# Performance work log

Measured on AMD Instinct MI355X. Metric: run time of the kernel, lower is better.

Reference implementation:

```python
import jax, jax.numpy as jnp
import numpy as np

HASH_PRIME = 5099  # primes[layer_id=0]
MIN_CAPACITY = 4


def setup_inputs() -> dict:
    key = jax.random.key(0)
    k1, k2, k3, k4, k5 = jax.random.split(key, 5)
    B, T, D, F, E = 8, 4096, 512, 1792, 64
    x = jax.random.normal(k1, (B, T, D), dtype=jnp.float32)
    token_ids = jax.random.randint(k2, (B, T), 0, 50257, dtype=jnp.int32)
    # Expert params stacked over E (random instead of the degenerate zero init)
    Wk = jax.random.normal(k3, (E, F, D), dtype=jnp.float32) * 0.02
    Wr = jax.random.normal(k4, (E, D, D), dtype=jnp.float32) * 0.02
    Wv = jax.random.normal(k5, (E, D, F), dtype=jnp.float32) * 0.02
    return {"x": x, "token_ids": token_ids, "Wk": Wk, "Wr": Wr, "Wv": Wv}


def reference(x, token_ids, Wk, Wr, Wv):
    B, T, D = x.shape
    E = Wk.shape[0]
    S = B * T
    # capacity_factor = 1, k = 1 -> capacity = ceil(S / E), at least min_capacity
    cap = max(MIN_CAPACITY, -(-S // E))

    tid = token_ids.reshape(S)
    e_idx = (tid % HASH_PRIME) % E                     # hash routing, top-1, gate weight 1.0

    onehot = jax.nn.one_hot(e_idx, E, dtype=jnp.int32)  # [S, E]
    rank = (jnp.cumsum(onehot, axis=0) * onehot).sum(axis=1)  # 1-based rank within expert
    pos = rank - 1                                      # slot index within expert
    kept = pos < cap                                    # capacity drop (first-come order)

    xf = x.reshape(S, D)
    pos_safe = jnp.where(kept, pos, cap)                # out-of-bounds -> dropped by scatter
    dispatched = jnp.zeros((E, cap, D), x.dtype).at[e_idx, pos_safe].set(xf, mode='drop')

    # RWKV expert FFN, batched over experts
    h = jnp.square(jax.nn.relu(jnp.einsum('ecd,efd->ecf', dispatched, Wk)))  # [E,C,F]
    kv = jnp.einsum('ecf,edf->ecd', h, Wv)                                   # [E,C,D]
    r = jax.nn.sigmoid(jnp.einsum('ecd,egd->ecg', dispatched, Wr))           # [E,C,D]
    expert_out = r * kv

    # combine: gather each token's slot; dropped tokens get zeros
    yf = expert_out[e_idx, jnp.minimum(pos, cap - 1)] * kept[:, None].astype(x.dtype)
    return yf.reshape(B, T, D)
```

## Files before the change

### kernel.cpp

```cpp
#include <hip/hip_runtime.h>
#include <hip/hip_fp16.h>

#define HASH_PRIME 5099
#define NE 64
#define ND 512
#define NF 1792
#define NS 32768
#define CAP 512

typedef unsigned short u16;
typedef __attribute__((ext_vector_type(8))) short bf16x8;
typedef __attribute__((ext_vector_type(4))) float f32x4;

__device__ __forceinline__ u16 f2bf(float f) {
  union { float f; unsigned u; } v; v.f = f;
  return (u16)((v.u + 0x7FFFu + ((v.u >> 16) & 1u)) >> 16);
}
__device__ __forceinline__ unsigned pkbf2(float a, float b) {
  return (unsigned)f2bf(a) | ((unsigned)f2bf(b) << 16);
}

__device__ __forceinline__ void gld16(const void* g, void* l) {
  __builtin_amdgcn_global_load_lds(
      (const __attribute__((address_space(1))) unsigned int*)(uintptr_t)g,
      (__attribute__((address_space(3))) unsigned int*)(uintptr_t)l,
      16, 0, 0);
}

__global__ __launch_bounds__(512) void route1(const int* __restrict__ tok,
                                              int* __restrict__ rank_local,
                                              int* __restrict__ hist) {
  __shared__ int se[512];
  __shared__ int h[NE];
  int b = blockIdx.x, t = threadIdx.x;
  int s = b * 512 + t;
  int e = (tok[s] % HASH_PRIME) % NE;
  se[t] = e;
  if (t < NE) h[t] = 0;
  __syncthreads();
  int cnt = 0;
  for (int j = 0; j < t; ++j) cnt += (se[j] == e);
  rank_local[s] = cnt;
  atomicAdd(&h[e], 1);
  __syncthreads();
  if (t < NE) hist[b * NE + t] = h[t];
}

__global__ __launch_bounds__(512) void route2(const int* __restrict__ tok,
                                              const int* __restrict__ rank_local,
                                              const int* __restrict__ hist,
                                              int* __restrict__ slot_src) {
  __shared__ int off[NE];
  int b = blockIdx.x, t = threadIdx.x;
  if (t < NE) {
    int o = 0;
    for (int bb = 0; bb < b; ++bb) o += hist[bb * NE + t];
    off[t] = o;
  }
  __syncthreads();
  int s = b * 512 + t;
  int e = (tok[s] % HASH_PRIME) % NE;
  int pos = off[e] + rank_local[s];
  if (pos < CAP) slot_src[e * CAP + pos] = s;
}

__global__ __launch_bounds__(256) void dispatchx(const float* __restrict__ x,
                                                 const int* __restrict__ slot_src,
                                                 u16* __restrict__ Xd) {
  int b = blockIdx.x;
  int t = threadIdx.x;
  int row = b * 4 + (t >> 6);
  int col = (t & 63) * 8;
  int s = slot_src[row];
  uint4 w = make_uint4(0u, 0u, 0u, 0u);
  if (s >= 0) {
    const float4* p = (const float4*)(x + (size_t)s * ND + col);
    float4 a = p[0], c = p[1];
    w.x = pkbf2(a.x, a.y); w.y = pkbf2(a.z, a.w);
    w.z = pkbf2(c.x, c.y); w.w = pkbf2(c.z, c.w);
  }
  *(uint4*)(Xd + (size_t)row * ND + col) = w;
}


#define GDECL \
  __shared__ u16 As[2][256 * 32]; \
  __shared__ u16 Bs[2][128 * 32]; \
  const int t = threadIdx.x; \
  const int l = t & 63; \
  const int w = t >> 6; \
  const int wm = w >> 1; \
  const int wn = w & 1; \
  const int lrow = l & 15; \
  const int swz = ((l >> 4) ^ ((l >> 1) & 3)) * 8; \
  const int ra_row = t >> 2; \
  const int ra_col = ((t & 3) ^ ((t >> 3) & 3)) * 8; \
  const int brow = t >> 2; \
  const int bseg = t & 3; \
  const int wb_idx = brow * 32 + (((t & 3) ^ ((t >> 3) & 3)) * 8);

#define INIT_ACC do { \
  _Pragma("unroll") for (int m_ = 0; m_ < 4; ++m_) \
    _Pragma("unroll") for (int n_ = 0; n_ < 4; ++n_) \
      acc[m_][n_] = (f32x4){0.f, 0.f, 0.f, 0.f}; \
} while (0)

#define ISSUE_A(buf, ks, abase, astride) do { \
  const u16* g_ = (abase) + (size_t)ra_row * (astride) + (ks) * 32 + ra_col; \
  gld16(g_, (char*)As[buf] + t * 16); \
  gld16(g_ + (size_t)128 * (astride), (char*)As[buf] + t * 16 + 8192); \
} while (0)

#define LOAD_B(ks, bbase, bstride) do { \
  const float4* p_ = (const float4*)((bbase) + (size_t)brow * (bstride) + (ks) * 32 + bseg * 8); \
  fb0 = p_[0]; fb1 = p_[1]; \
} while (0)

#define WRITE_B(buf) do { \
  uint4 wv_; \
  wv_.x = pkbf2(fb0.x, fb0.y); wv_.y = pkbf2(fb0.z, fb0.w); \
  wv_.z = pkbf2(fb1.x, fb1.y); wv_.w = pkbf2(fb1.z, fb1.w); \
  *(uint4*)&Bs[buf][wb_idx] = wv_; \
} while (0)

#define COMPUTE(buf) do { \
  bf16x8 af_[4], bf_[4]; \
  _Pragma("unroll") for (int m_ = 0; m_ < 4; ++m_) \
    af_[m_] = *(const bf16x8*)&As[buf][(wm * 64 + m_ * 16 + lrow) * 32 + swz]; \
  _Pragma("unroll") for (int n_ = 0; n_ < 4; ++n_) \
    bf_[n_] = *(const bf16x8*)&Bs[buf][(wn * 64 + n_ * 16 + lrow) * 32 + swz]; \
  _Pragma("unroll") for (int m_ = 0; m_ < 4; ++m_) \
    _Pragma("unroll") for (int n_ = 0; n_ < 4; ++n_) \
      acc[m_][n_] = __builtin_amdgcn_mfma_f32_16x16x32_bf16(af_[m_], bf_[n_], acc[m_][n_], 0, 0, 0); \
} while (0)

#define GEMM_LOOP(NK, abase, astride, bbase, bstride) do { \
  float4 fb0, fb1; \
  ISSUE_A(0, 0, abase, astride); \
  LOAD_B(0, bbase, bstride); \
  WRITE_B(0); \
  __syncthreads(); \
  _Pragma("unroll 2") \
  for (int ks = 0; ks < (NK); ++ks) { \
    const int cur = ks & 1; \
    if (ks + 1 < (NK)) { \
      ISSUE_A(cur ^ 1, ks + 1, abase, astride); \
      LOAD_B(ks + 1, bbase, bstride); \
    } \
    COMPUTE(cur); \
    if (ks + 1 < (NK)) WRITE_B(cur ^ 1); \
    __syncthreads(); \
  } \
} while (0)

__global__ __launch_bounds__(512, 4) void g1(const u16* __restrict__ Xd,
                                             const float* __restrict__ Wk,
                                             u16* __restrict__ H) {
  GDECL
  const int wg = (blockIdx.x & 7) * (1792 / 8) + (blockIdx.x >> 3);
  const int e = wg / 28, rem = wg % 28;
  const int n0 = (rem >> 1) * 128;
  const int m0 = (rem & 1) * 256;
  f32x4 acc[4][4];
  INIT_ACC;
  const u16*  abase = Xd + ((size_t)e * CAP + m0) * ND;
  const float* bbase = Wk + ((size_t)e * NF + n0) * ND;
  GEMM_LOOP(16, abase, ND, bbase, ND);

  #pragma unroll
  for (int m = 0; m < 4; ++m) {
    #pragma unroll
    for (int i = 0; i < 4; ++i) {
      int r = m0 + wm * 64 + m * 16 + (l >> 4) * 4 + i;
      size_t base = ((size_t)e * CAP + r) * NF + n0 + wn * 64 + lrow;
      #pragma unroll
      for (int n = 0; n < 4; ++n) {
        float v = acc[m][n][i];
        v = v > 0.f ? v * v : 0.f;
        H[base + n * 16] = f2bf(v);
      }
    }
  }
}

__global__ __launch_bounds__(512, 4) void g2a(const u16* __restrict__ Xd,
                                              const float* __restrict__ Wr,
                                              __half* __restrict__ R) {
  GDECL
  const int wg = (blockIdx.x & 7) * (512 / 8) + (blockIdx.x >> 3);
  const int e = wg / 8, rem = wg % 8;
  const int n0 = (rem >> 1) * 128;
  const int m0 = (rem & 1) * 256;
  f32x4 acc[4][4];
  INIT_ACC;
  const u16*  abase = Xd + ((size_t)e * CAP + m0) * ND;
  const float* bbase = Wr + ((size_t)e * ND + n0) * ND;
  GEMM_LOOP(16, abase, ND, bbase, ND);

  #pragma unroll
  for (int m = 0; m < 4; ++m) {
    #pragma unroll
    for (int i = 0; i < 4; ++i) {
      int r = m0 + wm * 64 + m * 16 + (l >> 4) * 4 + i;
      size_t base = ((size_t)e * CAP + r) * ND + n0 + wn * 64 + lrow;
      #pragma unroll
      for (int n = 0; n < 4; ++n) {
        float s = 1.f / (1.f + __expf(-acc[m][n][i]));
        R[base + n * 16] = __float2half(s);
      }
    }
  }
}

__global__ __launch_bounds__(512, 4) void g2b(const u16* __restrict__ H,
                                              const float* __restrict__ Wv,
                                              const __half* __restrict__ R,
                                              const int* __restrict__ slot_src,
                                              float* __restrict__ out) {
  GDECL
  __shared__ int ss[256];
  const int wg = (blockIdx.x & 7) * (512 / 8) + (blockIdx.x >> 3);
  const int e = wg / 8, rem = wg % 8;
  const int n0 = (rem >> 1) * 128;
  const int m0 = (rem & 1) * 256;
  if (t < 256) ss[t] = slot_src[e * CAP + m0 + t];
  f32x4 acc[4][4];
  INIT_ACC;
  const u16*  abase = H  + ((size_t)e * CAP + m0) * NF;
  const float* bbase = Wv + ((size_t)e * ND + n0) * NF;
  GEMM_LOOP(56, abase, NF, bbase, NF);

  #pragma unroll
  for (int m = 0; m < 4; ++m) {
    #pragma unroll
    for (int i = 0; i < 4; ++i) {
      int rl = wm * 64 + m * 16 + (l >> 4) * 4 + i;
      int s = ss[rl];
      if (s >= 0) {
        const __half* rp = R + ((size_t)e * CAP + m0 + rl) * ND + n0 + wn * 64 + lrow;
        float* op = out + (size_t)s * ND + n0 + wn * 64 + lrow;
        #pragma unroll
        for (int n = 0; n < 4; ++n) {
          op[n * 16] = __half2float(rp[n * 16]) * acc[m][n][i];
        }
      }
    }
  }
}

extern "C" void kernel_launch(void* const* d_in, const int* in_sizes, int n_in,
                              void* d_out, int out_size, void* d_ws, size_t ws_size,
                              hipStream_t stream) {
  const float* x   = (const float*)d_in[0];
  const int*   tok = (const int*)d_in[1];
  const float* Wk  = (const float*)d_in[2];
  const float* Wr  = (const float*)d_in[3];
  const float* Wv  = (const float*)d_in[4];
  float* out = (float*)d_out;

  char* ws = (char*)d_ws;
  int*    slot_src   = (int*)ws;
  int*    rank_local = (int*)(ws + 131072);
  int*    hist       = (int*)(ws + 262144);
  u16*    Xd         = (u16*)(ws + (1 << 20));
  __half* R          = (__half*)(ws + 34603008);
  u16*    H          = (u16*)(ws + 68157440);

  (void)hipMemsetAsync(d_out, 0, (size_t)out_size * sizeof(float), stream);
  (void)hipMemsetAsync(slot_src, 0xFF, NE * CAP * sizeof(int), stream);
  route1<<<64, 512, 0, stream>>>(tok, rank_local, hist);
  route2<<<64, 512, 0, stream>>>(tok, rank_local, hist, slot_src);
  dispatchx<<<NS / 4, 256, 0, stream>>>(x, slot_src, Xd);
  g1 <<<1792, 512, 0, stream>>>(Xd, Wk, H);
  g2a<<<512,  512, 0, stream>>>(Xd, Wr, R);
  g2b<<<512,  512, 0, stream>>>(H, Wv, R, slot_src, out);
}
```

Measured before the change: 343.5 us.

## Fuse receptance GEMM into value GEMM and shrink GEMM tiles to 128x128

Merges the Wr sigmoid GEMM into the Wv GEMM kernel. The sigmoid gate is kept packed as fp16 in registers, so the R intermediate is never written to or reread from global memory, and one launch is removed. Tiles change from 256x128 with 512 threads to 128x128 with 256 threads, with each thread loading 16 B-floats, which doubles the block counts. The trade-off is higher register pressure from holding the gate values across the second GEMM, plus more redundant weight loads because of the smaller M tiles.

```diff
diff --git a/kernel.cpp b/kernel.cpp
--- a/kernel.cpp
+++ b/kernel.cpp
@@ -18,6 +18,14 @@
 }
 __device__ __forceinline__ unsigned pkbf2(float a, float b) {
   return (unsigned)f2bf(a) | ((unsigned)f2bf(b) << 16);
+}
+__device__ __forceinline__ unsigned pkh2(float a, float b) {
+  __half2 h = __floats2half2_rn(a, b);
+  return __builtin_bit_cast(unsigned, h);
+}
+__device__ __forceinline__ float uph(unsigned w, int hi) {
+  __half2 h = __builtin_bit_cast(__half2, w);
+  return hi ? __high2float(h) : __low2float(h);
 }
 
 __device__ __forceinline__ void gld16(const void* g, void* l) {
@@ -84,7 +92,7 @@
 
 
 #define GDECL \
-  __shared__ u16 As[2][256 * 32]; \
+  __shared__ u16 As[2][128 * 32]; \
   __shared__ u16 Bs[2][128 * 32]; \
   const int t = threadIdx.x; \
   const int l = t & 63; \
@@ -95,9 +103,10 @@
   const int swz = ((l >> 4) ^ ((l >> 1) & 3)) * 8; \
   const int ra_row = t >> 2; \
   const int ra_col = ((t & 3) ^ ((t >> 3) & 3)) * 8; \
-  const int brow = t >> 2; \
-  const int bseg = t & 3; \
-  const int wb_idx = brow * 32 + (((t & 3) ^ ((t >> 3) & 3)) * 8);
+  const int brow_ = t >> 1; \
+  const int bseg = t & 1; \
+  const int wb0 = brow_ * 32 + (((bseg * 2)     ^ ((t >> 2) & 3)) * 8); \
+  const int wb1 = brow_ * 32 + (((bseg * 2 + 1) ^ ((t >> 2) & 3)) * 8);
 
 #define INIT_ACC do { \
   _Pragma("unroll") for (int m_ = 0; m_ < 4; ++m_) \
@@ -108,19 +117,22 @@
 #define ISSUE_A(buf, ks, abase, astride) do { \
   const u16* g_ = (abase) + (size_t)ra_row * (astride) + (ks) * 32 + ra_col; \
   gld16(g_, (char*)As[buf] + t * 16); \
-  gld16(g_ + (size_t)128 * (astride), (char*)As[buf] + t * 16 + 8192); \
+  gld16(g_ + (size_t)64 * (astride), (char*)As[buf] + t * 16 + 4096); \
 } while (0)
 
 #define LOAD_B(ks, bbase, bstride) do { \
-  const float4* p_ = (const float4*)((bbase) + (size_t)brow * (bstride) + (ks) * 32 + bseg * 8); \
-  fb0 = p_[0]; fb1 = p_[1]; \
+  const float4* p_ = (const float4*)((bbase) + (size_t)brow_ * (bstride) + (ks) * 32 + bseg * 16); \
+  fb0 = p_[0]; fb1 = p_[1]; fb2 = p_[2]; fb3 = p_[3]; \
 } while (0)
 
 #define WRITE_B(buf) do { \
-  uint4 wv_; \
-  wv_.x = pkbf2(fb0.x, fb0.y); wv_.y = pkbf2(fb0.z, fb0.w); \
-  wv_.z = pkbf2(fb1.x, fb1.y); wv_.w = pkbf2(fb1.z, fb1.w); \
-  *(uint4*)&Bs[buf][wb_idx] = wv_; \
+  uint4 w0_, w1_; \
+  w0_.x = pkbf2(fb0.x, fb0.y); w0_.y = pkbf2(fb0.z, fb0.w); \
+  w0_.z = pkbf2(fb1.x, fb1.y); w0_.w = pkbf2(fb1.z, fb1.w); \
+  w1_.x = pkbf2(fb2.x, fb2.y); w1_.y = pkbf2(fb2.z, fb2.w); \
+  w1_.z = pkbf2(fb3.x, fb3.y); w1_.w = pkbf2(fb3.z, fb3.w); \
+  *(uint4*)&Bs[buf][wb0] = w0_; \
+  *(uint4*)&Bs[buf][wb1] = w1_; \
 } while (0)
 
 #define COMPUTE(buf) do { \
@@ -135,7 +147,7 @@
 } while (0)
 
 #define GEMM_LOOP(NK, abase, astride, bbase, bstride) do { \
-  float4 fb0, fb1; \
+  float4 fb0, fb1, fb2, fb3; \
   ISSUE_A(0, 0, abase, astride); \
   LOAD_B(0, bbase, bstride); \
   WRITE_B(0); \
@@ -153,17 +165,17 @@
   } \
 } while (0)
 
-__global__ __launch_bounds__(512, 4) void g1(const u16* __restrict__ Xd,
+__global__ __launch_bounds__(256, 4) void g1(const u16* __restrict__ Xd,
                                              const float* __restrict__ Wk,
                                              u16* __restrict__ H) {
   GDECL
-  const int wg = (blockIdx.x & 7) * (1792 / 8) + (blockIdx.x >> 3);
-  const int e = wg / 28, rem = wg % 28;
-  const int n0 = (rem >> 1) * 128;
-  const int m0 = (rem & 1) * 256;
+  const int wg = (blockIdx.x & 7) * 448 + (blockIdx.x >> 3);
+  const int e = wg / 56, rem = wg % 56;
+  const int m0 = (rem & 3) * 128;
+  const int n0 = (rem >> 2) * 128;
   f32x4 acc[4][4];
   INIT_ACC;
-  const u16*  abase = Xd + ((size_t)e * CAP + m0) * ND;
+  const u16*   abase = Xd + ((size_t)e * CAP + m0) * ND;
   const float* bbase = Wk + ((size_t)e * NF + n0) * ND;
   GEMM_LOOP(16, abase, ND, bbase, ND);
 
@@ -183,52 +195,48 @@
   }
 }
 
-__global__ __launch_bounds__(512, 4) void g2a(const u16* __restrict__ Xd,
-                                              const float* __restrict__ Wr,
-                                              __half* __restrict__ R) {
+__global__ __launch_bounds__(256, 4) void g2(const u16* __restrict__ Xd,
+                                             const float* __restrict__ Wr,
+                                             const u16* __restrict__ H,
+                                             const float* __restrict__ Wv,
+                                             const int* __restrict__ slot_src,
+                                             float* __restrict__ out) {
   GDECL
-  const int wg = (blockIdx.x & 7) * (512 / 8) + (blockIdx.x >> 3);
-  const int e = wg / 8, rem = wg % 8;
-  const int n0 = (rem >> 1) * 128;
-  const int m0 = (rem & 1) * 256;
+  __shared__ int ss[128];
+  const int wg = (blockIdx.x & 7) * 128 + (blockIdx.x >> 3);
+  const int e = wg >> 4, rem = wg & 15;
+  const int m0 = (rem & 3) * 128;
+  const int n0 = (rem >> 2) * 128;
+  if (t < 128) ss[t] = slot_src[e * CAP + m0 + t];
   f32x4 acc[4][4];
+
   INIT_ACC;
-  const u16*  abase = Xd + ((size_t)e * CAP + m0) * ND;
-  const float* bbase = Wr + ((size_t)e * ND + n0) * ND;
-  GEMM_LOOP(16, abase, ND, bbase, ND);
-
+  {
+    const u16*   abase = Xd + ((size_t)e * CAP + m0) * ND;
+    const float* bbase = Wr + ((size_t)e * ND + n0) * ND;
+    GEMM_LOOP(16, abase, ND, bbase, ND);
+  }
+
+  unsigned rpk[4][4][2];
   #pragma unroll
   for (int m = 0; m < 4; ++m) {
     #pragma unroll
-    for (int i = 0; i < 4; ++i) {
-      int r = m0 + wm * 64 + m * 16 + (l >> 4) * 4 + i;
-      size_t base = ((size_t)e * CAP + r) * ND + n0 + wn * 64 + lrow;
-      #pragma unroll
-      for (int n = 0; n < 4; ++n) {
-        float s = 1.f / (1.f + __expf(-acc[m][n][i]));
-        R[base + n * 16] = __float2half(s);
-      }
+    for (int n = 0; n < 4; ++n) {
+      float r0 = 1.f / (1.f + __expf(-acc[m][n][0]));
+      float r1 = 1.f / (1.f + __expf(-acc[m][n][1]));
+      float r2 = 1.f / (1.f + __expf(-acc[m][n][2]));
+      float r3 = 1.f / (1.f + __expf(-acc[m][n][3]));
+      rpk[m][n][0] = pkh2(r0, r1);
+      rpk[m][n][1] = pkh2(r2, r3);
     }
   }
-}
-
-__global__ __launch_bounds__(512, 4) void g2b(const u16* __restrict__ H,
-                                              const float* __restrict__ Wv,
-                                              const __half* __restrict__ R,
-                                              const int* __restrict__ slot_src,
-                                              float* __restrict__ out) {
-  GDECL
-  __shared__ int ss[256];
-  const int wg = (blockIdx.x & 7) * (512 / 8) + (blockIdx.x >> 3);
-  const int e = wg / 8, rem = wg % 8;
-  const int n0 = (rem >> 1) * 128;
-  const int m0 = (rem & 1) * 256;
-  if (t < 256) ss[t] = slot_src[e * CAP + m0 + t];
-  f32x4 acc[4][4];
+
   INIT_ACC;
-  const u16*  abase = H  + ((size_t)e * CAP + m0) * NF;
-  const float* bbase = Wv + ((size_t)e * ND + n0) * NF;
-  GEMM_LOOP(56, abase, NF, bbase, NF);
+  {
+    const u16*   abase = H  + ((size_t)e * CAP + m0) * NF;
+    const float* bbase = Wv + ((size_t)e * ND + n0) * NF;
+    GEMM_LOOP(56, abase, NF, bbase, NF);
+  }
 
   #pragma unroll
   for (int m = 0; m < 4; ++m) {
@@ -237,11 +245,10 @@
       int rl = wm * 64 + m * 16 + (l >> 4) * 4 + i;
       int s = ss[rl];
       if (s >= 0) {
-        const __half* rp = R + ((size_t)e * CAP + m0 + rl) * ND + n0 + wn * 64 + lrow;
         float* op = out + (size_t)s * ND + n0 + wn * 64 + lrow;
         #pragma unroll
         for (int n = 0; n < 4; ++n) {
-          op[n * 16] = __half2float(rp[n * 16]) * acc[m][n][i];
+          op[n * 16] = uph(rpk[m][n][i >> 1], i & 1) * acc[m][n][i];
         }
       }
     }
@@ -263,15 +270,13 @@
   int*    rank_local = (int*)(ws + 131072);
   int*    hist       = (int*)(ws + 262144);
   u16*    Xd         = (u16*)(ws + (1 << 20));
-  __half* R          = (__half*)(ws + 34603008);
-  u16*    H          = (u16*)(ws + 68157440);
+  u16*    Hbuf       = (u16*)(ws + 68157440);
 
   (void)hipMemsetAsync(d_out, 0, (size_t)out_size * sizeof(float), stream);
   (void)hipMemsetAsync(slot_src, 0xFF, NE * CAP * sizeof(int), stream);
   route1<<<64, 512, 0, stream>>>(tok, rank_local, hist);
   route2<<<64, 512, 0, stream>>>(tok, rank_local, hist, slot_src);
   dispatchx<<<NS / 4, 256, 0, stream>>>(x, slot_src, Xd);
-  g1 <<<1792, 512, 0, stream>>>(Xd, Wk, H);
-  g2a<<<512,  512, 0, stream>>>(Xd, Wr, R);
-  g2b<<<512,  512, 0, stream>>>(H, Wv, R, slot_src, out);
-}
+  g1<<<3584, 256, 0, stream>>>(Xd, Wk, Hbuf);
+  g2<<<1024, 256, 0, stream>>>(Xd, Wr, Hbuf, Wv, slot_src, out);
+}
```

New measurement: 430.2 us. +25.3%, slower.
